# Kernel optimization log

Hardware: AMD Instinct MI355X
Metric: run time of the kernel (lower is better)

Reference implementation:

```python
import jax, jax.numpy as jnp
import numpy as np

D_MODEL = 768
NUM_HEADS = 12
D_K = D_MODEL // NUM_HEADS
B, S = 2, 2048


def setup_inputs() -> dict:
    key = jax.random.key(0)
    ks = jax.random.split(key, 7)
    scale = 1.0 / np.sqrt(D_MODEL)
    return {
        "query": jax.random.normal(ks[0], (B, S, D_MODEL), jnp.float32),
        "key_in": jax.random.normal(ks[1], (B, S, D_MODEL), jnp.float32),
        "value": jax.random.normal(ks[2], (B, S, D_MODEL), jnp.float32),
        # nn.Linear weights are [out, in]; y = x @ W.T
        "Wq": jax.random.normal(ks[3], (D_MODEL, D_MODEL), jnp.float32) * scale,
        "Wk": jax.random.normal(ks[4], (D_MODEL, D_MODEL), jnp.float32) * scale,
        "Wv": jax.random.normal(ks[5], (D_MODEL, D_MODEL), jnp.float32) * scale,
        "Wo": jax.random.normal(ks[6], (D_MODEL, D_MODEL), jnp.float32) * scale,
    }


def _split_heads(x):
    b, s, _ = x.shape
    return x.reshape(b, s, NUM_HEADS, D_K).transpose(0, 2, 1, 3)  # [B,H,S,Dk]


def reference(query, key_in, value, Wq, Wk, Wv, Wo):
    Q = _split_heads(query @ Wq.T)
    K = _split_heads(key_in @ Wk.T)
    V = _split_heads(value @ Wv.T)
    scores = jnp.einsum("bhqd,bhkd->bhqk", Q, K) / jnp.sqrt(jnp.float32(D_K))
    attn = jax.nn.softmax(scores, axis=-1)
    ctx = jnp.einsum("bhqk,bhkd->bhqd", attn, V)  # [B,H,S,Dk]
    ctx = ctx.transpose(0, 2, 1, 3).reshape(query.shape[0], query.shape[1], D_MODEL)
    return ctx @ Wo.T
```

## Files before the change

kernel.cpp:

```cpp
#include <hip/hip_runtime.h>
#include <hip/hip_bf16.h>


typedef __bf16 bf16x8 __attribute__((ext_vector_type(8)));
typedef float f32x4 __attribute__((ext_vector_type(4)));
typedef unsigned short u16;
typedef unsigned int u32;
typedef u16 u16x8 __attribute__((ext_vector_type(8)));
typedef u16 u16x4 __attribute__((ext_vector_type(4)));

#define SEQ 2048
#define DM  768
#define NH  12
#define DK  64
#define NBH 24
#define MTOT 4096
#define NEL 3145728
#define NWL 589824

__device__ __forceinline__ u16 f2b(float v) {
  __bf16 t = (__bf16)v;
  return __builtin_bit_cast(u16, t);
}

__device__ __forceinline__ void gl_lds16(const u16* g, u16* l) {
  __builtin_amdgcn_global_load_lds(
      (const __attribute__((address_space(1))) void*)g,
      (__attribute__((address_space(3))) void*)l, 16, 0, 0);
}

__device__ __forceinline__ int pos32(int k) {
  return (k < 16) ? (((k >> 2) << 3) + (k & 3))
                  : ((((k & 15) >> 2) << 3) + (k & 3) + 4);
}


__global__ __launch_bounds__(256) void to_bf16(
    const float* __restrict__ s0, const float* __restrict__ s1, const float* __restrict__ s2,
    const float* __restrict__ s3, const float* __restrict__ s4, const float* __restrict__ s5,
    const float* __restrict__ s6, u16* __restrict__ Xb, u16* __restrict__ Wb)
{
  size_t c = (size_t)blockIdx.x * 256 + threadIdx.x;
  const float* src;
  u16* dst;
  if (c < 1179648) {
    int seg = (int)(c / 393216);
    size_t off = (c % 393216) * 8;
    src = (seg == 0 ? s0 : seg == 1 ? s1 : s2) + off;
    dst = Xb + (size_t)seg * NEL + off;
  } else {
    size_t c2 = c - 1179648;
    int seg = (int)(c2 / 73728);
    size_t off = (c2 % 73728) * 8;
    src = (seg == 0 ? s3 : seg == 1 ? s4 : seg == 2 ? s5 : s6) + off;
    dst = Wb + (size_t)seg * NWL + off;
  }
  float4 f0 = *(const float4*)(src);
  float4 f1 = *(const float4*)(src + 4);
  u16x8 o;
  o[0] = f2b(f0.x); o[1] = f2b(f0.y); o[2] = f2b(f0.z); o[3] = f2b(f0.w);
  o[4] = f2b(f1.x); o[5] = f2b(f1.y); o[6] = f2b(f1.z); o[7] = f2b(f1.w);
  *(u16x8*)dst = o;
}

__device__ __forceinline__ void gemm2_core(
    const u16* __restrict__ X, const u16* __restrict__ W, void* __restrict__ Y,
    int m0, int n0, int mode, u16* As, u16* Bs)
{
  const int tid  = threadIdx.x;
  const int lane = tid & 63, w = tid >> 6;
  const int l15  = lane & 15, quad = lane >> 4;
  const int wm   = (w & 1) * 64, wn = (w >> 1) * 64;

  f32x4 acc[4][4] = {};

  for (int k0 = 0; k0 < DM; k0 += 32) {
    __syncthreads();
#pragma unroll
    for (int i = 0; i < 2; i++) {
      int c = i * 256 + tid;
      int row = c >> 2, cc = c & 3;
      gl_lds16(X + (size_t)(m0 + row) * DM + k0 + cc * 8, As + c * 8);
      gl_lds16(W + (size_t)(n0 + row) * DM + k0 + cc * 8, Bs + c * 8);
    }
    __syncthreads();
    bf16x8 af[4], bf[4];
#pragma unroll
    for (int t = 0; t < 4; t++) {
      af[t] = *(const bf16x8*)(&As[(wm + t * 16 + l15) * 32 + quad * 8]);
      bf[t] = *(const bf16x8*)(&Bs[(wn + t * 16 + l15) * 32 + quad * 8]);
    }
#pragma unroll
    for (int mt = 0; mt < 4; mt++)
#pragma unroll
      for (int nt = 0; nt < 4; nt++)
        acc[mt][nt] = __builtin_amdgcn_mfma_f32_16x16x32_bf16(af[mt], bf[nt], acc[mt][nt], 0, 0, 0);
  }

  if (mode == 2) {
    float* O = (float*)Y;
#pragma unroll
    for (int mt = 0; mt < 4; mt++) {
      int mg = m0 + wm + mt * 16 + quad * 4;
#pragma unroll
      for (int nt = 0; nt < 4; nt++) {
        int j = n0 + wn + nt * 16 + l15;
#pragma unroll
        for (int r = 0; r < 4; r++)
          O[(size_t)(mg + r) * DM + j] = acc[mt][nt][r];
      }
    }
  } else if (mode == 1) {
    u16* O = (u16*)Y;
#pragma unroll
    for (int mt = 0; mt < 4; mt++) {
      int mg = m0 + wm + mt * 16 + quad * 4;
      int b = mg >> 11, s = mg & 2047;
      int sp = (s & ~31) | pos32(s & 31);
#pragma unroll
      for (int nt = 0; nt < 4; nt++) {
        int j = n0 + wn + nt * 16 + l15;
        int h = j >> 6, d = j & 63;
        u16x4 o;
#pragma unroll
        for (int r = 0; r < 4; r++) o[r] = f2b(acc[mt][nt][r]);
        *(u16x4*)&O[((size_t)(b * NH + h) * DK + d) * SEQ + sp] = o;
      }
    }
  } else {
    u16* O = (u16*)Y;
#pragma unroll
    for (int mt = 0; mt < 4; mt++) {
      int mg = m0 + wm + mt * 16 + quad * 4;
#pragma unroll
      for (int nt = 0; nt < 4; nt++) {
        int j = n0 + wn + nt * 16 + l15;
        int h = j >> 6, d = j & 63;
#pragma unroll
        for (int r = 0; r < 4; r++) {
          int m = mg + r;
          int b = m >> 11, s = m & 2047;
          O[((size_t)(b * NH + h) * SEQ + s) * DK + d] = f2b(acc[mt][nt][r]);
        }
      }
    }
  }
}

__global__ __launch_bounds__(256) void qkv2(
    const u16* __restrict__ Xb, const u16* __restrict__ Wb,
    u16* __restrict__ Qhm, u16* __restrict__ Khm, u16* __restrict__ Vt)
{
  __shared__ __align__(16) u16 As[128 * 32];
  __shared__ __align__(16) u16 Bs[128 * 32];
  int mat = blockIdx.z;
  const u16* X = Xb + (size_t)mat * NEL;
  const u16* W = Wb + (size_t)mat * NWL;
  void* Y = (mat == 0) ? (void*)Qhm : (mat == 1) ? (void*)Khm : (void*)Vt;
  gemm2_core(X, W, Y, blockIdx.y * 128, blockIdx.x * 128, (mat == 2) ? 1 : 0, As, Bs);
}

__global__ __launch_bounds__(256) void bt2(
    const u16* __restrict__ Ctx, const u16* __restrict__ Wob, float* __restrict__ Y)
{
  __shared__ __align__(16) u16 As[128 * 32];
  __shared__ __align__(16) u16 Bs[128 * 32];
  gemm2_core(Ctx, Wob, Y, blockIdx.y * 128, blockIdx.x * 128, 2, As, Bs);
}

__global__ __launch_bounds__(256) void attn2(
    const u16* __restrict__ Qh, const u16* __restrict__ Kh,
    const u16* __restrict__ Vt, u16* __restrict__ ctx)
{
  __shared__ __align__(16) u16 smem[2 * 64 * 72];
  __shared__ float Ls[64];
  u16* Ks = smem;
  u16* Vs = smem + 64 * 72;

  const int tid  = threadIdx.x;
  const int lane = tid & 63, w = tid >> 6;
  const int l15  = lane & 15, quad = lane >> 4;
  const int qh = w & 1, kh = w >> 1;
  const int qt = blockIdx.x, bh = blockIdx.y;
  const int b = bh / NH, h = bh % NH;

  const u16* Qb = Qh + (size_t)bh * SEQ * DK;
  const u16* Kb = Kh + (size_t)bh * SEQ * DK;
  const u16* Vb = Vt + (size_t)bh * DK * SEQ;
  const int q0 = qt * 64 + qh * 32;

  bf16x8 qf[2][2];
#pragma unroll
  for (int QT = 0; QT < 2; QT++)
#pragma unroll
    for (int dk = 0; dk < 2; dk++)
      qf[QT][dk] = *(const bf16x8*)&Qb[(size_t)(q0 + QT * 16 + l15) * DK + dk * 32 + quad * 8];

  float lpart[2] = {0.f, 0.f};
  f32x4 oacc[4][2] = {};

  for (int kt = 0; kt < SEQ; kt += 64) {
    __syncthreads();
#pragma unroll
    for (int i = 0; i < 4; i++) {
      int c = i * 256 + tid;
      if (c < 512) {
        int key = c >> 3, c8 = c & 7;
        *(float4*)&Ks[key * 72 + c8 * 8] =
            *(const float4*)&Kb[(size_t)(kt + key) * DK + c8 * 8];
      } else {
        int cc = c - 512;
        int d = cc >> 3, c8 = cc & 7;
        *(float4*)&Vs[d * 72 + c8 * 8] =
            *(const float4*)&Vb[(size_t)d * SEQ + kt + c8 * 8];
      }
    }
    __syncthreads();

    f32x4 sc[2][2] = {};
#pragma unroll
    for (int MT = 0; MT < 2; MT++)
#pragma unroll
      for (int dk = 0; dk < 2; dk++) {
        bf16x8 kf = *(const bf16x8*)&Ks[(kh * 32 + MT * 16 + l15) * 72 + dk * 32 + quad * 8];
        sc[MT][0] = __builtin_amdgcn_mfma_f32_16x16x32_bf16(kf, qf[0][dk], sc[MT][0], 0, 0, 0);
        sc[MT][1] = __builtin_amdgcn_mfma_f32_16x16x32_bf16(kf, qf[1][dk], sc[MT][1], 0, 0, 0);
      }

    bf16x8 pf[2];
#pragma unroll
    for (int QT = 0; QT < 2; QT++) {
#pragma unroll
      for (int j = 0; j < 8; j++) {
        float s = sc[j >> 2][QT][j & 3] * 0.125f;
        float p = __expf(fminf(s, 30.0f));
        lpart[QT] += p;
        pf[QT][j] = (__bf16)p;
      }
    }

#pragma unroll
    for (int DT = 0; DT < 4; DT++) {
      bf16x8 vf = *(const bf16x8*)&Vs[(DT * 16 + l15) * 72 + kh * 32 + quad * 8];
      oacc[DT][0] = __builtin_amdgcn_mfma_f32_16x16x32_bf16(vf, pf[0], oacc[DT][0], 0, 0, 0);
      oacc[DT][1] = __builtin_amdgcn_mfma_f32_16x16x32_bf16(vf, pf[1], oacc[DT][1], 0, 0, 0);
    }
  }

  __syncthreads();

  float lw[2];
#pragma unroll
  for (int QT = 0; QT < 2; QT++) {
    float l = lpart[QT];
    l += __shfl_xor(l, 16);
    l += __shfl_xor(l, 32);
    lw[QT] = l;
  }

  float* Os = (float*)smem;
  float* Ob = Os + qh * (32 * 68);
  if (kh == 1) {
#pragma unroll
    for (int DT = 0; DT < 4; DT++)
#pragma unroll
      for (int QT = 0; QT < 2; QT++)
        *(f32x4*)&Ob[(QT * 16 + l15) * 68 + DT * 16 + quad * 4] = oacc[DT][QT];
    if (quad == 0) {
      Ls[qh * 32 + l15]      = lw[0];
      Ls[qh * 32 + 16 + l15] = lw[1];
    }
  }
  __syncthreads();
  if (kh == 0) {
#pragma unroll
    for (int QT = 0; QT < 2; QT++) {
      float inv = 1.0f / (lw[QT] + Ls[qh * 32 + QT * 16 + l15]);
      int s = q0 + QT * 16 + l15;
#pragma unroll
      for (int DT = 0; DT < 4; DT++) {
        f32x4 add = *(const f32x4*)&Ob[(QT * 16 + l15) * 68 + DT * 16 + quad * 4];
        u16x4 ov;
#pragma unroll
        for (int r = 0; r < 4; r++)
          ov[r] = f2b((oacc[DT][QT][r] + add[r]) * inv);
        *(u16x4*)&ctx[((size_t)(b * SEQ + s)) * DM + h * DK + DT * 16 + quad * 4] = ov;
      }
    }
  }
}


__device__ __forceinline__ void stage8(u16* dst, const void* src, size_t elemIdx, int isf32) {
  if (isf32) {
    const float* s = (const float*)src + elemIdx;
    float4 f0 = *(const float4*)(s);
    float4 f1 = *(const float4*)(s + 4);
    u16x8 o;
    o[0] = f2b(f0.x); o[1] = f2b(f0.y); o[2] = f2b(f0.z); o[3] = f2b(f0.w);
    o[4] = f2b(f1.x); o[5] = f2b(f1.y); o[6] = f2b(f1.z); o[7] = f2b(f1.w);
    *(u16x8*)dst = o;
  } else {
    *(float4*)dst = *(const float4*)((const u16*)src + elemIdx);
  }
}

__device__ __forceinline__ void gemm_core_fb(
    const void* __restrict__ X, const void* __restrict__ W, void* __restrict__ Y,
    int m0, int n0, int out_mode, u16* As, u16* Bs, int xf32, int wf32)
{
  const int tid  = threadIdx.x;
  const int lane = tid & 63, w = tid >> 6;
  const int l15  = lane & 15, quad = lane >> 4;
  const int wm   = (w & 1) * 64, wn = (w >> 1) * 64;
  f32x4 acc[4][4] = {};
  for (int k0 = 0; k0 < DM; k0 += 32) {
    __syncthreads();
#pragma unroll
    for (int i = 0; i < 2; i++) {
      int c = i * 256 + tid;
      int row = c >> 2, cc = c & 3;
      stage8(&As[c * 8], X, (size_t)(m0 + row) * DM + k0 + cc * 8, xf32);
      stage8(&Bs[c * 8], W, (size_t)(n0 + row) * DM + k0 + cc * 8, wf32);
    }
    __syncthreads();
    bf16x8 af[4], bf[4];
#pragma unroll
    for (int t = 0; t < 4; t++) {
      af[t] = *(const bf16x8*)(&As[(wm + t * 16 + l15) * 32 + quad * 8]);
      bf[t] = *(const bf16x8*)(&Bs[(wn + t * 16 + l15) * 32 + quad * 8]);
    }
#pragma unroll
    for (int mt = 0; mt < 4; mt++)
#pragma unroll
      for (int nt = 0; nt < 4; nt++)
        acc[mt][nt] = __builtin_amdgcn_mfma_f32_16x16x32_bf16(af[mt], bf[nt], acc[mt][nt], 0, 0, 0);
  }
  if (out_mode == 2) {
    float* O = (float*)Y;
#pragma unroll
    for (int mt = 0; mt < 4; mt++) {
      int mg = m0 + wm + mt * 16 + quad * 4;
#pragma unroll
      for (int nt = 0; nt < 4; nt++) {
        int j = n0 + wn + nt * 16 + l15;
#pragma unroll
        for (int r = 0; r < 4; r++)
          O[(size_t)(mg + r) * DM + j] = acc[mt][nt][r];
      }
    }
  } else {
    u16* O = (u16*)Y;
#pragma unroll
    for (int mt = 0; mt < 4; mt++) {
      int mg = m0 + wm + mt * 16 + quad * 4;
#pragma unroll
      for (int nt = 0; nt < 4; nt++) {
        int j = n0 + wn + nt * 16 + l15;
        int h = j >> 6, d = j & 63;
#pragma unroll
        for (int r = 0; r < 4; r++) {
          int m = mg + r;
          int b = m >> 11, s = m & 2047;
          O[((size_t)(b * NH + h) * SEQ + s) * DK + d] = f2b(acc[mt][nt][r]);
        }
      }
    }
  }
}

__global__ __launch_bounds__(256) void fb_qkv_gemm(
    const float* __restrict__ Xq, const float* __restrict__ Xk, const float* __restrict__ Xv,
    const float* __restrict__ Wq, const float* __restrict__ Wk, const float* __restrict__ Wv,
    u16* __restrict__ Yq, u16* __restrict__ Yk, u16* __restrict__ Yv)
{
  __shared__ __align__(16) u16 As[128 * 32];
  __shared__ __align__(16) u16 Bs[128 * 32];
  int mat = blockIdx.z;
  const float* X = (mat == 0) ? Xq : (mat == 1) ? Xk : Xv;
  const float* W = (mat == 0) ? Wq : (mat == 1) ? Wk : Wv;
  u16*         Y = (mat == 0) ? Yq : (mat == 1) ? Yk : Yv;
  gemm_core_fb(X, W, Y, blockIdx.y * 128, blockIdx.x * 128, 0, As, Bs, 1, 1);
}

__global__ __launch_bounds__(256) void fb_gemm_bt(
    const u16* __restrict__ X, const float* __restrict__ W, float* __restrict__ Y)
{
  __shared__ __align__(16) u16 As[128 * 32];
  __shared__ __align__(16) u16 Bs[128 * 32];
  gemm_core_fb(X, W, Y, blockIdx.y * 128, blockIdx.x * 128, 2, As, Bs, 0, 1);
}

__global__ __launch_bounds__(256) void fb_attn(
    const u16* __restrict__ Qh, const u16* __restrict__ Kh,
    const u16* __restrict__ Vh, u16* __restrict__ ctx)
{
  __shared__ __align__(16) u16 Ks[32 * 88];
  __shared__ __align__(16) u16 Vs[64 * 40];
  __shared__ __align__(16) u16 Ps[4][16 * 32];
  const int tid  = threadIdx.x;
  const int lane = tid & 63, w = tid >> 6;
  const int l15  = lane & 15, quad = lane >> 4;
  const int qt = blockIdx.x, bh = blockIdx.y;
  const int b = bh / NH, h = bh % NH;
  const u16* Qb = Qh + (size_t)bh * SEQ * DK;
  const u16* Kb = Kh + (size_t)bh * SEQ * DK;
  const u16* Vb = Vh + (size_t)bh * SEQ * DK;
  const int q0 = qt * 64 + w * 16;
  bf16x8 qf[2];
#pragma unroll
  for (int kk = 0; kk < 2; kk++)
    qf[kk] = *(const bf16x8*)(&Qb[(size_t)(q0 + l15) * DK + kk * 32 + quad * 8]);
  float m_i[4] = {-INFINITY, -INFINITY, -INFINITY, -INFINITY};
  float l_i[4] = {0.f, 0.f, 0.f, 0.f};
  f32x4 acc[4] = {};
  for (int kt = 0; kt < SEQ; kt += 32) {
    __syncthreads();
    {
      int c = tid;
      int row = c >> 3, c8 = c & 7;
      *(float4*)(&Ks[row * 88 + c8 * 8]) =
          *(const float4*)(&Kb[(size_t)(kt + row) * DK + c8 * 8]);
    }
#pragma unroll
    for (int i = 0; i < 4; i++) {
      int e = i * 256 + tid;
      int k = e >> 5, d2 = e & 31;
      u32 v = *(const u32*)(&Vb[(size_t)(kt + k) * DK + d2 * 2]);
      Vs[(d2 * 2)     * 40 + k] = (u16)(v & 0xffffu);
      Vs[(d2 * 2 + 1) * 40 + k] = (u16)(v >> 16);
    }
    __syncthreads();
    f32x4 sc[2] = {};
#pragma unroll
    for (int ktt = 0; ktt < 2; ktt++)
#pragma unroll
      for (int dk = 0; dk < 2; dk++) {
        bf16x8 kf = *(const bf16x8*)(&Ks[(ktt * 16 + l15) * 88 + dk * 32 + quad * 8]);
        sc[ktt] = __builtin_amdgcn_mfma_f32_16x16x32_bf16(qf[dk], kf, sc[ktt], 0, 0, 0);
      }
    float alph[4];
#pragma unroll
    for (int r = 0; r < 4; r++) {
      float s0 = sc[0][r] * 0.125f;
      float s1 = sc[1][r] * 0.125f;
      float mv = fmaxf(s0, s1);
      mv = fmaxf(mv, __shfl_xor(mv, 1));
      mv = fmaxf(mv, __shfl_xor(mv, 2));
      mv = fmaxf(mv, __shfl_xor(mv, 4));
      mv = fmaxf(mv, __shfl_xor(mv, 8));
      float mnew = fmaxf(m_i[r], mv);
      float a = __expf(m_i[r] - mnew);
      m_i[r] = mnew;
      float p0 = __expf(s0 - mnew);
      float p1 = __expf(s1 - mnew);
      float rs = p0 + p1;
      rs += __shfl_xor(rs, 1);
      rs += __shfl_xor(rs, 2);
      rs += __shfl_xor(rs, 4);
      rs += __shfl_xor(rs, 8);
      l_i[r] = l_i[r] * a + rs;
      alph[r] = a;
      Ps[w][(quad * 4 + r) * 32 +      l15] = f2b(p0);
      Ps[w][(quad * 4 + r) * 32 + 16 + l15] = f2b(p1);
    }
#pragma unroll
    for (int nt = 0; nt < 4; nt++) {
      acc[nt][0] *= alph[0];
      acc[nt][1] *= alph[1];
      acc[nt][2] *= alph[2];
      acc[nt][3] *= alph[3];
    }
    __syncthreads();
    bf16x8 pf = *(const bf16x8*)(&Ps[w][l15 * 32 + quad * 8]);
#pragma unroll
    for (int nt = 0; nt < 4; nt++) {
      bf16x8 vf = *(const bf16x8*)(&Vs[(nt * 16 + l15) * 40 + quad * 8]);
      acc[nt] = __builtin_amdgcn_mfma_f32_16x16x32_bf16(pf, vf, acc[nt], 0, 0, 0);
    }
  }
#pragma unroll
  for (int nt = 0; nt < 4; nt++) {
    int d = nt * 16 + l15;
#pragma unroll
    for (int r = 0; r < 4; r++) {
      int s = q0 + quad * 4 + r;
      float v = acc[nt][r] / l_i[r];
      ctx[((size_t)(b * SEQ + s)) * DM + h * DK + d] = f2b(v);
    }
  }
}


extern "C" void kernel_launch(void* const* d_in, const int* in_sizes, int n_in,
                              void* d_out, int out_size, void* d_ws, size_t ws_size,
                              hipStream_t stream) {
  const float* act[3] = {nullptr, nullptr, nullptr};
  const float* wgt[4] = {nullptr, nullptr, nullptr, nullptr};
  int na = 0, nw = 0;
  for (int i = 0; i < n_in && i < 7; i++) {
    if (in_sizes[i] == NEL) { if (na < 3) act[na++] = (const float*)d_in[i]; }
    else                    { if (nw < 4) wgt[nw++] = (const float*)d_in[i]; }
  }
  const float* q  = act[0] ? act[0] : (const float*)d_in[0];
  const float* k  = act[1] ? act[1] : (const float*)d_in[1];
  const float* v  = act[2] ? act[2] : (const float*)d_in[2];
  const float* Wq = wgt[0] ? wgt[0] : (const float*)d_in[3];
  const float* Wk = wgt[1] ? wgt[1] : (const float*)d_in[4];
  const float* Wv = wgt[2] ? wgt[2] : (const float*)d_in[5];
  const float* Wo = wgt[3] ? wgt[3] : (const float*)d_in[6];
  u16* ws = (u16*)d_ws;

  const size_t NE = NEL, NW = NWL;
  const size_t need = (6 * NE + 4 * NW) * 2;

  if (ws_size >= need) {
    u16* Xb  = ws;
    u16* Wb  = ws + 3 * NE;
    u16* Qhm = Wb + 4 * NW;
    u16* Khm = Qhm + NE;
    u16* Vt  = Khm + NE;
    u16* Ctx = ws;

    to_bf16<<<5760, 256, 0, stream>>>(q, k, v, Wq, Wk, Wv, Wo, Xb, Wb);
    qkv2<<<dim3(DM / 128, MTOT / 128, 3), 256, 0, stream>>>(Xb, Wb, Qhm, Khm, Vt);
    attn2<<<dim3(SEQ / 64, NBH), 256, 0, stream>>>(Qhm, Khm, Vt, Ctx);
    bt2<<<dim3(DM / 128, MTOT / 128), 256, 0, stream>>>(Ctx, Wb + 3 * NW, (float*)d_out);
  } else {
    u16* Qhm = ws;
    u16* Khm = ws + NE;
    u16* Vhm = ws + 2 * NE;
    u16* Ctx = ws + 3 * NE;
    fb_qkv_gemm<<<dim3(DM / 128, MTOT / 128, 3), 256, 0, stream>>>(
        q, k, v, Wq, Wk, Wv, Qhm, Khm, Vhm);
    fb_attn<<<dim3(SEQ / 64, NBH), 256, 0, stream>>>(Qhm, Khm, Vhm, Ctx);
    fb_gemm_bt<<<dim3(DM / 128, MTOT / 128), 256, 0, stream>>>(Ctx, Wo, (float*)d_out);
  }
}
```

Before: 200.7 us.

## Double K-tile depth with XOR-swizzled LDS in GEMMs and attention, stage Q/K epilogue

The GEMM core now loads 64-wide K slices per barrier pair, using an XOR swizzle on the LDS layout to avoid bank conflicts. The Q/K head-major epilogue is staged through LDS so each output row is written with 16-byte stores instead of scalar 2-byte stores. The attention kernel processes 128 keys per iteration and fills K/V tiles with direct global-to-LDS loads into swizzled layouts. This cuts barrier count and uncoalesced writes at the cost of more shared memory per block, which may lower occupancy.

```diff
diff --git a/kernel.cpp b/kernel.cpp
--- a/kernel.cpp
+++ b/kernel.cpp
@@ -74,27 +74,32 @@
 
   f32x4 acc[4][4] = {};
 
-  for (int k0 = 0; k0 < DM; k0 += 32) {
-    __syncthreads();
-#pragma unroll
-    for (int i = 0; i < 2; i++) {
-      int c = i * 256 + tid;
-      int row = c >> 2, cc = c & 3;
-      gl_lds16(X + (size_t)(m0 + row) * DM + k0 + cc * 8, As + c * 8);
-      gl_lds16(W + (size_t)(n0 + row) * DM + k0 + cc * 8, Bs + c * 8);
-    }
-    __syncthreads();
-    bf16x8 af[4], bf[4];
-#pragma unroll
-    for (int t = 0; t < 4; t++) {
-      af[t] = *(const bf16x8*)(&As[(wm + t * 16 + l15) * 32 + quad * 8]);
-      bf[t] = *(const bf16x8*)(&Bs[(wn + t * 16 + l15) * 32 + quad * 8]);
-    }
-#pragma unroll
-    for (int mt = 0; mt < 4; mt++)
-#pragma unroll
-      for (int nt = 0; nt < 4; nt++)
-        acc[mt][nt] = __builtin_amdgcn_mfma_f32_16x16x32_bf16(af[mt], bf[nt], acc[mt][nt], 0, 0, 0);
+  for (int k0 = 0; k0 < DM; k0 += 64) {
+    __syncthreads();
+#pragma unroll
+    for (int i = 0; i < 4; i++) {
+      int c = (w * 4 + i) * 64 + lane;
+      int row = c >> 3, c8 = c & 7;
+      int g8 = c8 ^ (row & 7);
+      gl_lds16(X + (size_t)(m0 + row) * DM + k0 + g8 * 8, As + c * 8);
+      gl_lds16(W + (size_t)(n0 + row) * DM + k0 + g8 * 8, Bs + c * 8);
+    }
+    __syncthreads();
+#pragma unroll
+    for (int dk = 0; dk < 2; dk++) {
+      bf16x8 af[4], bf[4];
+      int ph = ((dk * 4 + quad) ^ (l15 & 7)) * 8;
+#pragma unroll
+      for (int t = 0; t < 4; t++) {
+        af[t] = *(const bf16x8*)(&As[(wm + t * 16 + l15) * 64 + ph]);
+        bf[t] = *(const bf16x8*)(&Bs[(wn + t * 16 + l15) * 64 + ph]);
+      }
+#pragma unroll
+      for (int mt = 0; mt < 4; mt++)
+#pragma unroll
+        for (int nt = 0; nt < 4; nt++)
+          acc[mt][nt] = __builtin_amdgcn_mfma_f32_16x16x32_bf16(af[mt], bf[nt], acc[mt][nt], 0, 0, 0);
+    }
   }
 
   if (mode == 2) {
@@ -129,19 +134,30 @@
     }
   } else {
     u16* O = (u16*)Y;
-#pragma unroll
-    for (int mt = 0; mt < 4; mt++) {
-      int mg = m0 + wm + mt * 16 + quad * 4;
-#pragma unroll
-      for (int nt = 0; nt < 4; nt++) {
-        int j = n0 + wn + nt * 16 + l15;
-        int h = j >> 6, d = j & 63;
-#pragma unroll
-        for (int r = 0; r < 4; r++) {
-          int m = mg + r;
-          int b = m >> 11, s = m & 2047;
-          O[((size_t)(b * NH + h) * SEQ + s) * DK + d] = f2b(acc[mt][nt][r]);
-        }
+    u16* T = As;
+#pragma unroll
+    for (int h2 = 0; h2 < 2; h2++) {
+      __syncthreads();
+      if ((w & 1) == h2) {
+#pragma unroll
+        for (int mt = 0; mt < 4; mt++)
+#pragma unroll
+          for (int nt = 0; nt < 4; nt++)
+#pragma unroll
+            for (int r = 0; r < 4; r++)
+              T[(mt * 16 + quad * 4 + r) * 128 + wn + nt * 16 + l15] = f2b(acc[mt][nt][r]);
+      }
+      __syncthreads();
+#pragma unroll
+      for (int i = 0; i < 4; i++) {
+        int c = i * 256 + tid;
+        int row = c >> 4, ch = c & 15;
+        u16x8 val = *(const u16x8*)&T[row * 128 + ch * 8];
+        int m = m0 + h2 * 64 + row;
+        int j = n0 + ch * 8;
+        int hh = j >> 6, d = j & 63;
+        int b = m >> 11, s = m & 2047;
+        *(u16x8*)&O[((size_t)(b * NH + hh) * SEQ + s) * DK + d] = val;
       }
     }
   }
@@ -151,8 +167,8 @@
     const u16* __restrict__ Xb, const u16* __restrict__ Wb,
     u16* __restrict__ Qhm, u16* __restrict__ Khm, u16* __restrict__ Vt)
 {
-  __shared__ __align__(16) u16 As[128 * 32];
-  __shared__ __align__(16) u16 Bs[128 * 32];
+  __shared__ __align__(16) u16 As[128 * 64];
+  __shared__ __align__(16) u16 Bs[128 * 64];
   int mat = blockIdx.z;
   const u16* X = Xb + (size_t)mat * NEL;
   const u16* W = Wb + (size_t)mat * NWL;
@@ -163,8 +179,8 @@
 __global__ __launch_bounds__(256) void bt2(
     const u16* __restrict__ Ctx, const u16* __restrict__ Wob, float* __restrict__ Y)
 {
-  __shared__ __align__(16) u16 As[128 * 32];
-  __shared__ __align__(16) u16 Bs[128 * 32];
+  __shared__ __align__(16) u16 As[128 * 64];
+  __shared__ __align__(16) u16 Bs[128 * 64];
   gemm2_core(Ctx, Wob, Y, blockIdx.y * 128, blockIdx.x * 128, 2, As, Bs);
 }
 
@@ -172,10 +188,10 @@
     const u16* __restrict__ Qh, const u16* __restrict__ Kh,
     const u16* __restrict__ Vt, u16* __restrict__ ctx)
 {
-  __shared__ __align__(16) u16 smem[2 * 64 * 72];
+  __shared__ __align__(16) u16 smem[128 * 64 + 64 * 128];
   __shared__ float Ls[64];
   u16* Ks = smem;
-  u16* Vs = smem + 64 * 72;
+  u16* Vs = smem + 128 * 64;
 
   const int tid  = threadIdx.x;
   const int lane = tid & 63, w = tid >> 6;
@@ -199,51 +215,57 @@
   float lpart[2] = {0.f, 0.f};
   f32x4 oacc[4][2] = {};
 
-  for (int kt = 0; kt < SEQ; kt += 64) {
+  for (int kt = 0; kt < SEQ; kt += 128) {
     __syncthreads();
 #pragma unroll
     for (int i = 0; i < 4; i++) {
-      int c = i * 256 + tid;
-      if (c < 512) {
-        int key = c >> 3, c8 = c & 7;
-        *(float4*)&Ks[key * 72 + c8 * 8] =
-            *(const float4*)&Kb[(size_t)(kt + key) * DK + c8 * 8];
-      } else {
-        int cc = c - 512;
-        int d = cc >> 3, c8 = cc & 7;
-        *(float4*)&Vs[d * 72 + c8 * 8] =
-            *(const float4*)&Vb[(size_t)d * SEQ + kt + c8 * 8];
-      }
-    }
-    __syncthreads();
-
-    f32x4 sc[2][2] = {};
-#pragma unroll
-    for (int MT = 0; MT < 2; MT++)
+      int c = (w * 4 + i) * 64 + lane;
+      int row = c >> 3, c8 = c & 7;
+      gl_lds16(Kb + (size_t)(kt + row) * DK + (c8 ^ (row & 7)) * 8, Ks + c * 8);
+    }
+#pragma unroll
+    for (int i = 0; i < 4; i++) {
+      int c = (w * 4 + i) * 64 + lane;
+      int d = c >> 4, c16 = c & 15;
+      gl_lds16(Vb + (size_t)d * SEQ + kt + (c16 ^ (d & 15)) * 8, Vs + c * 8);
+    }
+    __syncthreads();
+
+    f32x4 sc[4][2] = {};
+#pragma unroll
+    for (int MT = 0; MT < 4; MT++) {
+      int row = kh * 64 + MT * 16 + l15;
 #pragma unroll
       for (int dk = 0; dk < 2; dk++) {
-        bf16x8 kf = *(const bf16x8*)&Ks[(kh * 32 + MT * 16 + l15) * 72 + dk * 32 + quad * 8];
+        bf16x8 kf = *(const bf16x8*)&Ks[row * 64 + ((dk * 4 + quad) ^ (l15 & 7)) * 8];
         sc[MT][0] = __builtin_amdgcn_mfma_f32_16x16x32_bf16(kf, qf[0][dk], sc[MT][0], 0, 0, 0);
         sc[MT][1] = __builtin_amdgcn_mfma_f32_16x16x32_bf16(kf, qf[1][dk], sc[MT][1], 0, 0, 0);
       }
-
-    bf16x8 pf[2];
-#pragma unroll
-    for (int QT = 0; QT < 2; QT++) {
-#pragma unroll
-      for (int j = 0; j < 8; j++) {
-        float s = sc[j >> 2][QT][j & 3] * 0.125f;
-        float p = __expf(fminf(s, 30.0f));
-        lpart[QT] += p;
-        pf[QT][j] = (__bf16)p;
-      }
-    }
-
-#pragma unroll
-    for (int DT = 0; DT < 4; DT++) {
-      bf16x8 vf = *(const bf16x8*)&Vs[(DT * 16 + l15) * 72 + kh * 32 + quad * 8];
-      oacc[DT][0] = __builtin_amdgcn_mfma_f32_16x16x32_bf16(vf, pf[0], oacc[DT][0], 0, 0, 0);
-      oacc[DT][1] = __builtin_amdgcn_mfma_f32_16x16x32_bf16(vf, pf[1], oacc[DT][1], 0, 0, 0);
+    }
+
+    bf16x8 pf[2][2];
+#pragma unroll
+    for (int QT = 0; QT < 2; QT++)
+#pragma unroll
+      for (int kk = 0; kk < 2; kk++)
+#pragma unroll
+        for (int j = 0; j < 8; j++) {
+          float s = sc[kk * 2 + (j >> 2)][QT][j & 3] * 0.125f;
+          float p = __expf(fminf(s, 30.0f));
+          lpart[QT] += p;
+          pf[kk][QT][j] = (__bf16)p;
+        }
+
+#pragma unroll
+    for (int kk = 0; kk < 2; kk++) {
+      int cL = kh * 8 + kk * 4 + quad;
+#pragma unroll
+      for (int DT = 0; DT < 4; DT++) {
+        int d = DT * 16 + l15;
+        bf16x8 vf = *(const bf16x8*)&Vs[d * 128 + (cL ^ (d & 15)) * 8];
+        oacc[DT][0] = __builtin_amdgcn_mfma_f32_16x16x32_bf16(vf, pf[kk][0], oacc[DT][0], 0, 0, 0);
+        oacc[DT][1] = __builtin_amdgcn_mfma_f32_16x16x32_bf16(vf, pf[kk][1], oacc[DT][1], 0, 0, 0);
+      }
     }
   }
 
```

Result: faster. 194.2 us (-3.2%).
